# Optimization experiments

Measured on AMD Instinct MI355X. Metric: run time of the kernel, lower is better.

The kernel has to match this reference:

```python
import jax, jax.numpy as jnp
import numpy as np

EPS = 1e-5

# The 8 fixed sobel kernels from the original module. Summing convolutions with
# the same input equals one convolution with the summed kernel, so we embed the
# four 3x3 kernels (pad=1) into 5x5 (pad=2) and precombine everything into a
# single depthwise 5x5 kernel (exactly the math of detect_edge_1/2 summed).
_K3 = [
    [[2, 4, 2], [0, 0, 0], [-2, -4, -2]],
    [[4, 2, 0], [2, 0, -2], [0, -2, -4]],
    [[2, 0, -2], [4, 0, -4], [2, 0, -2]],
    [[0, -2, -4], [2, 0, -2], [4, 2, 0]],
]
_K5 = [
    [[0, 0, 0, 0, 0], [0, -2, -4, -2, 0], [-1, -4, 0, 4, 1], [0, 2, 4, 2, 0], [0, 0, 0, 0, 0]],
    [[0, 0, -1, 0, 0], [0, -2, -4, 2, 0], [0, -4, 0, 4, 0], [0, -2, 4, 2, 0], [0, 0, 1, 0, 0]],
    [[0, 0, 1, 0, 0], [0, -2, 4, 2, 0], [0, -4, 0, 4, 0], [0, -2, -4, 2, 0], [0, 0, -1, 0, 0]],
    [[0, 0, 0, 0, 0], [0, 2, 4, 2, 0], [-1, -4, 0, 4, 1], [0, -2, -4, -2, 0], [0, 0, 0, 0, 0]],
]

def _combined_sobel_kernel():
    k = np.zeros((5, 5), dtype=np.float32)
    for k3 in _K3:
        k[1:4, 1:4] += np.asarray(k3, dtype=np.float32)
    for k5 in _K5:
        k += np.asarray(k5, dtype=np.float32)
    return jnp.asarray(k)

SOBEL_K = _combined_sobel_kernel()  # [5,5]


def _conv2d(x, w, b, pad):
    # x: [N,C,H,W], w: [O,I,kh,kw]
    y = jax.lax.conv_general_dilated(
        x, w, window_strides=(1, 1), padding=[(pad, pad), (pad, pad)],
        dimension_numbers=('NCHW', 'OIHW', 'NCHW'))
    return y + b[None, :, None, None]


def _bn_relu(y, gamma, beta):
    # BatchNorm2d in training mode: per-channel batch stats over (N,H,W),
    # biased variance, eps=1e-5.
    m = jnp.mean(y, axis=(0, 2, 3), keepdims=True)
    v = jnp.mean(jnp.square(y - m), axis=(0, 2, 3), keepdims=True)
    yn = (y - m) * jax.lax.rsqrt(v + EPS)
    return jax.nn.relu(yn * gamma[None, :, None, None] + beta[None, :, None, None])


def _single_conv(x, w, b, gamma, beta, pad):
    return _bn_relu(_conv2d(x, w, b, pad), gamma, beta)


def _sobel(x):
    # Fused depthwise conv replacing the per-channel loops over 8 kernels.
    C = x.shape[1]
    w = jnp.broadcast_to(SOBEL_K[None, None], (C, 1, 5, 5))
    return jax.lax.conv_general_dilated(
        x, w, window_strides=(1, 1), padding=[(2, 2), (2, 2)],
        dimension_numbers=('NCHW', 'OIHW', 'NCHW'), feature_group_count=C)


def setup_inputs() -> dict:
    key = jax.random.key(0)
    ks = jax.random.split(key, 16)
    Cin, Cout = 64, 128
    Ch = Cout // 2
    B, H, W = 8, 160, 160
    s = 0.05
    d = {
        'input_f': jax.random.normal(ks[0], (B, Cin, H, W), jnp.float32),
        'w1': jax.random.normal(ks[1], (Cout, Cin, 1, 1), jnp.float32) * s,
        'b1': jnp.zeros((Cout,), jnp.float32),
        'g1': jnp.ones((Cout,), jnp.float32),
        'be1': jnp.zeros((Cout,), jnp.float32),
        'w2': jax.random.normal(ks[2], (Ch, Cout, 3, 3), jnp.float32) * s,
        'b2': jnp.zeros((Ch,), jnp.float32),
        'g2': jnp.ones((Ch,), jnp.float32),
        'be2': jnp.zeros((Ch,), jnp.float32),
        'w3': jax.random.normal(ks[3], (Ch, Ch, 3, 3), jnp.float32) * s,
        'b3': jnp.zeros((Ch,), jnp.float32),
        'g3': jnp.ones((Ch,), jnp.float32),
        'be3': jnp.zeros((Ch,), jnp.float32),
        'w4': jax.random.normal(ks[4], (Ch, Cin, 3, 3), jnp.float32) * s,
        'b4': jnp.zeros((Ch,), jnp.float32),
        'g4': jnp.ones((Ch,), jnp.float32),
        'be4': jnp.zeros((Ch,), jnp.float32),
    }
    return d


def reference(input_f, w1, b1, g1, be1, w2, b2, g2, be2, w3, b3, g3, be3, w4, b4, g4, be4):
    c1 = _single_conv(input_f, w1, b1, g1, be1, pad=0)   # [B,Cout,H,W]
    c2 = _single_conv(c1, w2, b2, g2, be2, pad=1)        # [B,Cout//2,H,W]
    edge = _sobel(c2)                                    # depthwise sobel sum
    c3 = _single_conv(edge, w3, b3, g3, be3, pad=1)
    skip = _single_conv(input_f, w4, b4, g4, be4, pad=1)
    return jnp.concatenate([skip, c3], axis=1)           # [B,Cout,H,W]
```

## Files before the change

kernel.cpp:

```cpp
#include <hip/hip_runtime.h>

typedef unsigned short u16;
typedef unsigned int u32;
typedef __attribute__((ext_vector_type(8))) short bf16x8;
typedef __attribute__((ext_vector_type(4))) float f32x4;

#define WD 160
#define HW 25600
#define NPIXF 204800.0f
#define BNEPS 1e-5f
#define SLOTB 6553600ll
#define BATB  13107200ll

__device__ __forceinline__ float bf2f(u16 u){ return __uint_as_float(((u32)u)<<16); }
__device__ __forceinline__ u16 f2bf(float f){ u32 x=__float_as_uint(f); return (u16)((x + 0x7FFFu + ((x>>16)&1u))>>16); }
__device__ __forceinline__ u32 pack2(float a,float b){ return (u32)f2bf(a) | ((u32)f2bf(b)<<16); }

__device__ __forceinline__ f32x4 MF(bf16x8 a, bf16x8 b, f32x4 c){
  return __builtin_amdgcn_mfma_f32_16x16x32_bf16(a, b, c, 0, 0, 0);
}
__device__ __forceinline__ void gload16(const void* g, void* l){
  __builtin_amdgcn_global_load_lds((const __attribute__((address_space(1))) void*)(g),
                                   (__attribute__((address_space(3))) void*)(l), 16, 0, 0);
}

__global__ __launch_bounds__(256) void k_prepw(
    const float* __restrict__ w1, const float* __restrict__ w2,
    const float* __restrict__ w3, const float* __restrict__ w4,
    u16* __restrict__ wp1, u16* __restrict__ wp2,
    u16* __restrict__ wp3, u16* __restrict__ wp4)
{
  int t = blockIdx.x*256 + threadIdx.x;
  if (t < 8192){
    int i = t&7, oc = (t>>3)&127, kc = (t>>10)&3, icb = t>>12;
    wp1[t] = f2bf(w1[oc*64 + icb*32 + kc*8 + i]);
  }
  int u = t - 8192;
  if (u >= 0 && u < 73728){
    int i = u&7, oc = (u>>3)&63, kc = (u>>9)&3, v = u>>11;
    int icb = (v*57)>>9; int tap = v - icb*9;
    wp2[u] = f2bf(w2[(oc*128 + icb*32 + kc*8 + i)*9 + tap]);
  }
  int u3 = t - (8192+73728);
  if (u3 >= 0 && u3 < 36864){
    int k = u3&31, oc = (u3>>5)&63, v = u3>>11;
    int icb = (v >= 9) ? 1 : 0; int tap = v - icb*9;
    wp3[u3] = f2bf(w3[(oc*64 + icb*32 + k)*9 + tap]);
    wp4[u3] = f2bf(w4[(oc*64 + icb*32 + k)*9 + tap]);
  }
}

__global__ __launch_bounds__(256,4) void k_conv1(
    const float* __restrict__ x, const u16* __restrict__ wp1,
    char* __restrict__ dout, float* __restrict__ stats, int nslot)
{
  __shared__ __align__(16) char Xs[16384];
  const int tid = threadIdx.x, lane = tid&63, w = tid>>6;
  const int l15 = lane&15, kc = lane>>4;
  int flat = blockIdx.x + 200*blockIdx.y;
  flat = (flat&7)*200 + (flat>>3);
  const int b = flat/200, bx = flat - b*200;
  const int px0 = bx*128;
  const float* xb = x + (size_t)b*64*HW;

#pragma unroll
  for (int q=0; q<4; ++q){
    int s = q*256 + tid;
    int px = s & 127, ck = (s>>7)&3, icb = s>>9;
    const float* pb = xb + (size_t)(icb*32 + ck*8)*HW + px0 + px;
    u32 w4[4];
#pragma unroll
    for (int j=0;j<4;++j)
      w4[j] = pack2(pb[(size_t)(2*j)*HW], pb[(size_t)(2*j+1)*HW]);
    *(uint4*)(Xs + icb*8192 + px*64 + ((ck ^ ((px>>1)&3))<<4))
        = make_uint4(w4[0],w4[1],w4[2],w4[3]);
  }
  __syncthreads();

  f32x4 acc[4][4];
  for (int t=0;t<4;++t) for (int o=0;o<4;++o) acc[t][o] = (f32x4){0.f,0.f,0.f,0.f};
  const int och = (w>>1)*64;
  int a1off[4];
  for (int t=0;t<4;++t){
    int px = (w&1)*64 + t*16 + l15;
    a1off[t] = px*64 + ((kc ^ ((px>>1)&3))<<4);
  }
#pragma unroll
  for (int icb=0; icb<2; ++icb){
    bf16x8 a[4], bw[4];
#pragma unroll
    for (int t=0;t<4;++t) a[t] = *(const bf16x8*)(Xs + icb*8192 + a1off[t]);
#pragma unroll
    for (int o=0;o<4;++o)
      bw[o] = *(const bf16x8*)(wp1 + ((size_t)(icb*4 + kc)*128 + och + o*16 + l15)*8);
#pragma unroll
    for (int t=0;t<4;++t)
#pragma unroll
      for (int o=0;o<4;++o)
        acc[t][o] = MF(a[t], bw[o], acc[t][o]);
  }

  u16* c1 = (u16*)(dout + (size_t)b*BATB);
  float sa[4]={0,0,0,0}, sq[4]={0,0,0,0};
  for (int t=0;t<4;++t){
    int pxb = px0 + (w&1)*64 + t*16 + kc*4;
    for (int o=0;o<4;++o){
      int oc = och + o*16 + l15;
#pragma unroll
      for (int r=0;r<4;++r){
        float v = acc[t][o][r];
        c1[(size_t)(pxb + r)*128 + oc] = f2bf(v);
        sa[o]+=v; sq[o]+=v*v;
      }
    }
  }
  const int slot = flat & (nslot-1);
  for (int o=0;o<4;++o){
    float s1_=sa[o], s2_=sq[o];
    s1_+=__shfl_xor(s1_,16); s2_+=__shfl_xor(s2_,16);
    s1_+=__shfl_xor(s1_,32); s2_+=__shfl_xor(s2_,32);
    if (lane < 16){
      float* p = stats + ((size_t)slot*128 + och + o*16 + l15)*4;
      atomicAdd(p, s1_); atomicAdd(p+1, s2_);
    }
  }
}

__global__ void k_fold23(const float* __restrict__ s2, const float* __restrict__ s3,
                         float* __restrict__ f23, int nslot){
  int t = threadIdx.x;
  const float* src = (t < 128) ? s2 : s3;
  int c = t & 127;
  float sm=0.f, sq=0.f;
  for (int s=0;s<nslot;++s){ const float* p = src + ((size_t)s*128 + c)*4; sm+=p[0]; sq+=p[1]; }
  f23[t*2] = sm; f23[t*2+1] = sq;
}

__global__ __launch_bounds__(256,4) void k_conv2(
    char* __restrict__ dout, const u16* __restrict__ wp2,
    const float* __restrict__ S0, const float* __restrict__ g1,
    const float* __restrict__ be1,
    float* __restrict__ statsO, int nslot)
{
  __shared__ __align__(16) char Xs[21760];
  __shared__ __align__(16) float scbi[128][2];
  const int tid = threadIdx.x, lane = tid&63, w = tid>>6;
  const int l15 = lane&15, kc = lane>>4;
  int flat = blockIdx.x + 5*(blockIdx.y + 20*blockIdx.z);
  flat = (flat&7)*100 + (flat>>3);
  const int b = flat/100; int r100 = flat - b*100;
  const int by = r100/5, bx = r100 - by*5;
  const int gx0 = bx*32, gy0 = by*8;
  const u16* c1raw = (const u16*)(dout + (size_t)b*BATB);
  u16* raw2 = (u16*)(dout + (size_t)b*BATB + SLOTB);

  if (tid < 128){
    float sm=0.f, sq=0.f;
    for (int s=0;s<nslot;++s){ const float* p = S0 + ((size_t)s*128 + tid)*4; sm+=p[0]; sq+=p[1]; }
    float m = sm/NPIXF;
    float v = sq/NPIXF - m*m;
    float sc = g1[tid]*rsqrtf(v + BNEPS);
    scbi[tid][0] = sc; scbi[tid][1] = be1[tid] - m*sc;
  }

  f32x4 acc[4][4];
  for (int t=0;t<4;++t) for (int o=0;o<4;++o) acc[t][o] = (f32x4){0.f,0.f,0.f,0.f};

  int xon[2][3];
  for (int h=0;h<2;++h) for (int dx=0;dx<3;++dx){
    int xi = l15 + h*16 + dx;
    xon[h][dx] = xi*64 + ((kc ^ ((xi>>1)&3))<<4);
  }

  __syncthreads();
  for (int icb=0; icb<4; ++icb){
    if (icb) __syncthreads();
    for (int s = tid; s < 1360; s += 256){
      int p = s>>2, sub = s&3;
      int yy = (int)(((u32)p*241u)>>13);
      int xi = p - yy*34;
      int gy = gy0 - 1 + yy, gx = gx0 - 1 + xi;
      int c = sub ^ ((xi>>1)&3);
      uint4 o4 = make_uint4(0,0,0,0);
      if ((unsigned)gy < 160u && (unsigned)gx < 160u){
        int cb = icb*32 + c*8;
        uint4 q = *(const uint4*)(c1raw + ((size_t)(gy*WD+gx)*128 + cb));
        u32 ww[4] = {q.x,q.y,q.z,q.w};
        u32 ro[4];
#pragma unroll
        for (int j=0;j<4;++j){
          float lo = bf2f((u16)(ww[j]&0xFFFFu)), hi = bf2f((u16)(ww[j]>>16));
          lo = fmaxf(0.f, lo*scbi[cb+2*j][0]   + scbi[cb+2*j][1]);
          hi = fmaxf(0.f, hi*scbi[cb+2*j+1][0] + scbi[cb+2*j+1][1]);
          ro[j] = pack2(lo, hi);
        }
        o4 = make_uint4(ro[0],ro[1],ro[2],ro[3]);
      }
      *(uint4*)(Xs + p*64 + sub*16) = o4;
    }
    __syncthreads();
#pragma unroll
    for (int tap=0; tap<9; ++tap){
      const int dy = tap/3, dx = tap - dy*3;
      bf16x8 a[4], bw[4];
#pragma unroll
      for (int o=0;o<4;++o)
        bw[o] = *(const bf16x8*)(wp2 + ((size_t)((icb*9 + tap)*4 + kc)*64 + o*16 + l15)*8);
#pragma unroll
      for (int t=0;t<4;++t)
        a[t] = *(const bf16x8*)(Xs + (2*w + (t>>1) + dy)*2176 + xon[t&1][dx]);
#pragma unroll
      for (int t=0;t<4;++t)
#pragma unroll
        for (int o=0;o<4;++o)
          acc[t][o] = MF(a[t], bw[o], acc[t][o]);
    }
  }

  float sa[4]={0,0,0,0}, sq[4]={0,0,0,0};
  for (int t=0;t<4;++t){
    int gy = gy0 + 2*w + (t>>1);
    int gxb = gx0 + (t&1)*16 + kc*4;
    for (int o=0;o<4;++o){
      int oc = o*16 + l15;
#pragma unroll
      for (int r=0;r<4;++r){
        float v = acc[t][o][r];
        raw2[(size_t)(gy*WD + gxb + r)*64 + oc] = f2bf(v);
        sa[o]+=v; sq[o]+=v*v;
      }
    }
  }
  int slot = flat & (nslot-1);
  for (int o=0;o<4;++o){
    float s1_=sa[o], s2_=sq[o];
    s1_+=__shfl_xor(s1_,16); s2_+=__shfl_xor(s2_,16);
    s1_+=__shfl_xor(s1_,32); s2_+=__shfl_xor(s2_,32);
    if (lane<16){
      float* p = statsO + ((size_t)slot*128 + o*16 + l15)*4;
      atomicAdd(p,s1_); atomicAdd(p+1,s2_);
    }
  }
}

__global__ __launch_bounds__(256) void k_sobel(
    char* __restrict__ dout, const float* __restrict__ S1,
    const float* __restrict__ g2, const float* __restrict__ be2,
    u16* __restrict__ edge_base, long ebstride, int nslot)
{
  __shared__ float ascS[8], abiS[8];
  int tid = threadIdx.x;
  int b = blockIdx.z, cb = blockIdx.y;
  if (tid < 64){
    int c = cb*8 + (tid&7);
    float sm=0.f, sq=0.f;
    for (int s = tid>>3; s < nslot; s += 8){
      const float* p = S1 + ((size_t)s*128 + c)*4;
      sm += p[0]; sq += p[1];
    }
    sm += __shfl_xor(sm, 8);  sq += __shfl_xor(sq, 8);
    sm += __shfl_xor(sm, 16); sq += __shfl_xor(sq, 16);
    sm += __shfl_xor(sm, 32); sq += __shfl_xor(sq, 32);
    if (tid < 8){
      float m = sm/NPIXF, v = sq/NPIXF - m*m;
      float sc = g2[c]*rsqrtf(v+BNEPS);
      ascS[tid] = sc; abiS[tid] = be2[c] - m*sc;
    }
  }
  __syncthreads();
  int px = blockIdx.x*256 + tid;
  int y = (int)(((u32)px*52429u)>>23);
  int x = px - y*WD;
  const u16* raw2 = (const u16*)(dout + (size_t)b*BATB + SLOTB);
  u16* edge = edge_base + (size_t)b*ebstride;
  float av[8] = {0,0,0,0,0,0,0,0};
  auto TAP = [&](int dy, int dx, float wt){
    int yy = y+dy, xx = x+dx;
    if ((unsigned)yy>=160u || (unsigned)xx>=160u) return;
    uint4 q = *(const uint4*)(raw2 + ((size_t)(yy*WD+xx)*64 + cb*8));
    u32 ww[4] = {q.x,q.y,q.z,q.w};
#pragma unroll
    for (int j=0;j<4;++j){
      float lo = bf2f((u16)(ww[j]&0xFFFFu)), hi = bf2f((u16)(ww[j]>>16));
      lo = fmaxf(0.f, lo*ascS[2*j]   + abiS[2*j]);
      hi = fmaxf(0.f, hi*ascS[2*j+1] + abiS[2*j+1]);
      av[2*j]   += wt*lo;
      av[2*j+1] += wt*hi;
    }
  };
  TAP(-1,-1,4.f); TAP(-1,0,4.f);
  TAP(0,-2,-2.f); TAP(0,-1,-8.f); TAP(0,1,8.f); TAP(0,2,2.f);
  TAP(1,0,-4.f);  TAP(1,1,-4.f);
  uint4 o;
  o.x = pack2(av[0],av[1]); o.y = pack2(av[2],av[3]);
  o.z = pack2(av[4],av[5]); o.w = pack2(av[6],av[7]);
  *(uint4*)(edge + ((size_t)px*64 + cb*8)) = o;
}

__global__ __launch_bounds__(256,2) void k_conv34(
    char* __restrict__ dout, const float* __restrict__ x,
    const u16* __restrict__ wp3, const u16* __restrict__ wp4,
    float* __restrict__ st3, float* __restrict__ st4,
    const u16* __restrict__ zeros, const u16* __restrict__ edge_base,
    long ebstride, int nslot, int mode)
{
  __shared__ __align__(16) char Xs[24576];
  const int tid = threadIdx.x, lane = tid&63, w = tid>>6;
  const int l15 = lane&15, kc = lane>>4;
  int b, job;
  if (mode == 2){ b = blockIdx.z>>1; job = blockIdx.z&1; }
  else          { b = blockIdx.z;    job = mode; }
  const int gx0 = blockIdx.x*32, gy0 = blockIdx.y*8;
  const u16* wp = job ? wp4 : wp3;
  float* statsO = job ? st4 : st3;
  float* out = job ? (float*)(dout + (size_t)b*BATB)
                   : (float*)(dout + (size_t)b*BATB + SLOTB);
  const float* xb = x + (size_t)b*64*HW;
  const u16* edge = edge_base + (size_t)b*ebstride;

  f32x4 acc[4][4];
  for (int m=0;m<4;++m) for (int t=0;t<4;++t) acc[m][t] = (f32x4){0.f,0.f,0.f,0.f};
  int xon[2][3];
  for (int h=0;h<2;++h) for (int dx=0;dx<3;++dx){
    int xi = l15 + h*16 + dx;
    xon[h][dx] = xi*64 + ((kc ^ ((xi>>1)&3))<<4);
  }

  for (int icb=0; icb<2; ++icb){
    if (icb) __syncthreads();
    if (job){
      for (int s = tid; s < 1600; s += 256){
        int s10 = (int)(((u32)s*6554u)>>16);
        int q = s - s10*10;
        int cp = (int)(((u32)s10*6554u)>>16);
        int yq = s10 - cp*10;
        int gy = gy0 - 1 + yq;
        int gxq = gx0 - 4 + q*4;
        float fa[4] = {0,0,0,0}, fb[4] = {0,0,0,0};
        if ((unsigned)gy < 160u){
          const float* pa = xb + (size_t)(icb*32 + cp*2)*HW + gy*WD + gxq;
          if (gxq >= 0 && gxq + 3 < 160){
            float4 va = *(const float4*)pa;
            float4 vb = *(const float4*)(pa + HW);
            fa[0]=va.x; fa[1]=va.y; fa[2]=va.z; fa[3]=va.w;
            fb[0]=vb.x; fb[1]=vb.y; fb[2]=vb.z; fb[3]=vb.w;
          } else {
#pragma unroll
            for (int e=0;e<4;++e){
              int gx = gxq + e;
              if ((unsigned)gx < 160u){ fa[e] = pa[e]; fb[e] = pa[e + HW]; }
            }
          }
        }
#pragma unroll
        for (int e=0;e<4;++e){
          int xi = gxq + e - (gx0 - 1);
          if ((unsigned)xi < 34u){
            int phys = (yq*34 + xi)*64 + (((cp>>2) ^ ((xi>>1)&3))<<4) + (cp&3)*4;
            *(u32*)(Xs + phys) = pack2(fa[e], fb[e]);
          }
        }
      }
    } else {
      for (int it=0; it<6; ++it){
        int s = it*256 + tid;
        int p = s>>2, sub = s&3;
        int yy = (int)(((u32)p*241u)>>13);
        int xi = p - yy*34;
        int gy = gy0-1+yy, gx = gx0-1+xi;
        int c = sub ^ ((xi>>1)&3);
        const u16* src = zeros + ((tid&63)<<3);
        if (p<340 && (unsigned)gy<160u && (unsigned)gx<160u)
          src = edge + ((size_t)(gy*WD+gx)*64 + icb*32 + c*8);
        gload16(src, Xs + (it*256 + (tid & ~63))*16);
      }
      asm volatile("s_waitcnt vmcnt(0)" ::: "memory");
    }
    __syncthreads();

#pragma unroll
    for (int tap=0; tap<9; ++tap){
      const int dy = tap/3, dx = tap - dy*3;
      bf16x8 a[4], bv[4];
#pragma unroll
      for (int m=0;m<4;++m)
        a[m] = *(const bf16x8*)(wp + ((size_t)((icb*9+tap)*64 + m*16 + l15)*32 + kc*8));
#pragma unroll
      for (int t=0;t<4;++t)
        bv[t] = *(const bf16x8*)(Xs + (2*w + (t>>1) + dy)*2176 + xon[t&1][dx]);
#pragma unroll
      for (int m=0;m<4;++m)
#pragma unroll
        for (int t=0;t<4;++t)
          acc[m][t] = MF(a[m], bv[t], acc[m][t]);
    }
  }

  float sa[4][4], sq[4][4];
  for (int m=0;m<4;++m) for (int r=0;r<4;++r){ sa[m][r]=0.f; sq[m][r]=0.f; }
  for (int m=0;m<4;++m){
    for (int t=0;t<4;++t){
      int gy = gy0 + 2*w + (t>>1);
      int gx = gx0 + (t&1)*16 + l15;
#pragma unroll
      for (int r=0;r<4;++r){
        float v = acc[m][t][r];
        out[(size_t)(m*16 + kc*4 + r)*HW + gy*WD + gx] = v;
        sa[m][r]+=v; sq[m][r]+=v*v;
      }
    }
  }
  int slot = (blockIdx.x + 5*(blockIdx.y + 20*blockIdx.z)) & (nslot-1);
  for (int m=0;m<4;++m)
    for (int r=0;r<4;++r){
      float s1_=sa[m][r], s2_=sq[m][r];
      s1_+=__shfl_xor(s1_,1); s2_+=__shfl_xor(s2_,1);
      s1_+=__shfl_xor(s1_,2); s2_+=__shfl_xor(s2_,2);
      s1_+=__shfl_xor(s1_,4); s2_+=__shfl_xor(s2_,4);
      s1_+=__shfl_xor(s1_,8); s2_+=__shfl_xor(s2_,8);
      if (l15==0){
        float* p = statsO + ((size_t)slot*128 + m*16 + kc*4 + r)*4;
        atomicAdd(p,s1_); atomicAdd(p+1,s2_);
      }
    }
}

__global__ __launch_bounds__(256) void k_bnrelu(
    float* __restrict__ io, const float* __restrict__ f23,
    const float* __restrict__ g3, const float* __restrict__ be3,
    const float* __restrict__ g4, const float* __restrict__ be4)
{
  size_t e = ((size_t)blockIdx.x*256 + threadIdx.x)*8;
  int cg = (int)((e/HW) & 127);
  float* p = io + (size_t)blockIdx.y*3276800 + e;
  float sm,sq,gg,bb;
  if (cg>=64){ int c=cg-64; sm=f23[c*2]; sq=f23[c*2+1]; gg=g3[c]; bb=be3[c]; }
  else       { sm=f23[(128+cg)*2]; sq=f23[(128+cg)*2+1]; gg=g4[cg]; bb=be4[cg]; }
  float m = sm/NPIXF;
  float v = sq/NPIXF - m*m;
  float sc = gg*rsqrtf(v + BNEPS);
  float bi = bb - m*sc;
  float4 a = *(float4*)p;
  float4 bq = *(float4*)(p+4);
  a.x=fmaxf(0.f,a.x*sc+bi); a.y=fmaxf(0.f,a.y*sc+bi);
  a.z=fmaxf(0.f,a.z*sc+bi); a.w=fmaxf(0.f,a.w*sc+bi);
  bq.x=fmaxf(0.f,bq.x*sc+bi); bq.y=fmaxf(0.f,bq.y*sc+bi);
  bq.z=fmaxf(0.f,bq.z*sc+bi); bq.w=fmaxf(0.f,bq.w*sc+bi);
  *(float4*)p = a;
  *(float4*)(p+4) = bq;
}

extern "C" void kernel_launch(void* const* d_in, const int* in_sizes, int n_in,
                              void* d_out, int out_size, void* d_ws, size_t ws_size,
                              hipStream_t stream)
{
  const float* x   = (const float*)d_in[0];
  const float* w1  = (const float*)d_in[1];
  const float* g1  = (const float*)d_in[3];
  const float* be1 = (const float*)d_in[4];
  const float* w2  = (const float*)d_in[5];
  const float* g2  = (const float*)d_in[7];
  const float* be2 = (const float*)d_in[8];
  const float* w3  = (const float*)d_in[9];
  const float* g3  = (const float*)d_in[11];
  const float* be3 = (const float*)d_in[12];
  const float* w4  = (const float*)d_in[13];
  const float* g4  = (const float*)d_in[15];
  const float* be4 = (const float*)d_in[16];
  (void)in_sizes; (void)n_in; (void)out_size;

  int nslot = 32;
  auto need = [&](int ns)->size_t{
    return (size_t)4*ns*128*4*4 + 4096 + (size_t)(8192+73728+36864+36864)*2 + 1024;
  };
  while (nslot > 1 && need(nslot) > ws_size) nslot >>= 1;
  if (need(nslot) > ws_size) return;

  char* ws = (char*)d_ws;
  float* S = (float*)ws;
  size_t stg = (size_t)nslot*128*4;
  float* S0=S, *S1=S+stg, *S2=S+2*stg, *S3=S+3*stg;
  float* F = S + 4*stg;
  u16* wp1 = (u16*)(F + 1024);
  u16* wp2 = wp1 + 8192;
  u16* wp3 = wp2 + 73728;
  u16* wp4 = wp3 + 36864;
  u16* zeros = wp4 + 36864;
  size_t base = need(nslot);
  bool bigWS = (ws_size >= base + 26214400ull);
  u16* edge_base; long ebstride;
  if (bigWS){ edge_base = (u16*)(ws + base); ebstride = 64L*HW; }
  else      { edge_base = (u16*)((char*)d_out + 3276800); ebstride = BATB/2; }

  hipMemsetAsync(S, 0, 4*stg*sizeof(float), stream);
  hipMemsetAsync(zeros, 0, 1024, stream);

  k_prepw<<<464, 256, 0, stream>>>(w1, w2, w3, w4, wp1, wp2, wp3, wp4);
  k_conv1<<<dim3(200,8), 256, 0, stream>>>(x, wp1, (char*)d_out, S0, nslot);
  k_conv2<<<dim3(5,20,8), 256, 0, stream>>>((char*)d_out, wp2, S0, g1, be1, S1, nslot);
  k_sobel<<<dim3(100,8,8), 256, 0, stream>>>((char*)d_out, S1, g2, be2,
                                             edge_base, ebstride, nslot);
  if (bigWS){
    k_conv34<<<dim3(5,20,16), 256, 0, stream>>>((char*)d_out, x, wp3, wp4, S2, S3,
                                                zeros, edge_base, ebstride, nslot, 2);
  } else {
    k_conv34<<<dim3(5,20,8), 256, 0, stream>>>((char*)d_out, x, wp3, wp4, S2, S3,
                                               zeros, edge_base, ebstride, nslot, 0);
    k_conv34<<<dim3(5,20,8), 256, 0, stream>>>((char*)d_out, x, wp3, wp4, S2, S3,
                                               zeros, edge_base, ebstride, nslot, 1);
  }
  k_fold23<<<1, 256, 0, stream>>>(S2, S3, F, nslot);
  k_bnrelu<<<dim3(1600,8), 256, 0, stream>>>((float*)d_out, F, g3, be3, g4, be4);
}
```

Measured before the change: 341.6 us.

## Fuse skip conv with sobel into one launch, run conv3 alone

Adds a combined kernel whose first 800 blocks compute the skip-branch 3x3 conv (conv4) from the fp32 input with MFMA and accumulate BN stats. The remaining blocks perform the sobel edge computation. Because neither job depends on the other, they run concurrently within a single grid, and the later conv34 launch then only handles conv3. This aims to fill the GPU better and hide the memory-bound sobel behind compute-bound conv work, at the cost of more code and a larger mixed-role grid. It applies only on the large-workspace path.

```diff
diff --git a/kernel.cpp b/kernel.cpp
--- a/kernel.cpp
+++ b/kernel.cpp
@@ -295,6 +295,166 @@
   o.x = pack2(av[0],av[1]); o.y = pack2(av[2],av[3]);
   o.z = pack2(av[4],av[5]); o.w = pack2(av[6],av[7]);
   *(uint4*)(edge + ((size_t)px*64 + cb*8)) = o;
+}
+
+__global__ __launch_bounds__(256,2) void k_skipsobel(
+    char* __restrict__ dout, const float* __restrict__ x,
+    const u16* __restrict__ wp4, float* __restrict__ st4,
+    const float* __restrict__ S1, const float* __restrict__ g2,
+    const float* __restrict__ be2,
+    u16* __restrict__ edge_base, long ebstride, int nslot)
+{
+  __shared__ __align__(16) char Xs[24576];
+  __shared__ float ascS[8], abiS[8];
+  const int tid = threadIdx.x;
+  const int bid = blockIdx.x;
+
+  if (bid < 800){
+    const int lane = tid&63, w = tid>>6, l15 = lane&15, kc = lane>>4;
+    const int b = bid/100; int r100 = bid - b*100;
+    const int by = r100/5, bx = r100 - by*5;
+    const int gx0 = bx*32, gy0 = by*8;
+    const float* xb = x + (size_t)b*64*HW;
+    float* out = (float*)(dout + (size_t)b*BATB);
+
+    f32x4 acc[4][4];
+    for (int m=0;m<4;++m) for (int t=0;t<4;++t) acc[m][t] = (f32x4){0.f,0.f,0.f,0.f};
+    int xon[2][3];
+    for (int h=0;h<2;++h) for (int dx=0;dx<3;++dx){
+      int xi = l15 + h*16 + dx;
+      xon[h][dx] = xi*64 + ((kc ^ ((xi>>1)&3))<<4);
+    }
+
+    for (int icb=0; icb<2; ++icb){
+      if (icb) __syncthreads();
+      for (int s = tid; s < 1600; s += 256){
+        int s10 = (int)(((u32)s*6554u)>>16);
+        int q = s - s10*10;
+        int cp = (int)(((u32)s10*6554u)>>16);
+        int yq = s10 - cp*10;
+        int gy = gy0 - 1 + yq;
+        int gxq = gx0 - 4 + q*4;
+        float fa[4] = {0,0,0,0}, fb[4] = {0,0,0,0};
+        if ((unsigned)gy < 160u){
+          const float* pa = xb + (size_t)(icb*32 + cp*2)*HW + gy*WD + gxq;
+          if (gxq >= 0 && gxq + 3 < 160){
+            float4 va = *(const float4*)pa;
+            float4 vb = *(const float4*)(pa + HW);
+            fa[0]=va.x; fa[1]=va.y; fa[2]=va.z; fa[3]=va.w;
+            fb[0]=vb.x; fb[1]=vb.y; fb[2]=vb.z; fb[3]=vb.w;
+          } else {
+#pragma unroll
+            for (int e=0;e<4;++e){
+              int gx = gxq + e;
+              if ((unsigned)gx < 160u){ fa[e] = pa[e]; fb[e] = pa[e + HW]; }
+            }
+          }
+        }
+#pragma unroll
+        for (int e=0;e<4;++e){
+          int xi = gxq + e - (gx0 - 1);
+          if ((unsigned)xi < 34u){
+            int phys = (yq*34 + xi)*64 + (((cp>>2) ^ ((xi>>1)&3))<<4) + (cp&3)*4;
+            *(u32*)(Xs + phys) = pack2(fa[e], fb[e]);
+          }
+        }
+      }
+      __syncthreads();
+
+#pragma unroll
+      for (int tap=0; tap<9; ++tap){
+        const int dy = tap/3, dx = tap - dy*3;
+        bf16x8 a[4], bv[4];
+#pragma unroll
+        for (int m=0;m<4;++m)
+          a[m] = *(const bf16x8*)(wp4 + ((size_t)((icb*9+tap)*64 + m*16 + l15)*32 + kc*8));
+#pragma unroll
+        for (int t=0;t<4;++t)
+          bv[t] = *(const bf16x8*)(Xs + (2*w + (t>>1) + dy)*2176 + xon[t&1][dx]);
+#pragma unroll
+        for (int m=0;m<4;++m)
+#pragma unroll
+          for (int t=0;t<4;++t)
+            acc[m][t] = MF(a[m], bv[t], acc[m][t]);
+      }
+    }
+
+    float sa[4][4], sq[4][4];
+    for (int m=0;m<4;++m) for (int r=0;r<4;++r){ sa[m][r]=0.f; sq[m][r]=0.f; }
+    for (int m=0;m<4;++m){
+      for (int t=0;t<4;++t){
+        int gy = gy0 + 2*w + (t>>1);
+        int gx = gx0 + (t&1)*16 + l15;
+#pragma unroll
+        for (int r=0;r<4;++r){
+          float v = acc[m][t][r];
+          out[(size_t)(m*16 + kc*4 + r)*HW + gy*WD + gx] = v;
+          sa[m][r]+=v; sq[m][r]+=v*v;
+        }
+      }
+    }
+    int slot = bid & (nslot-1);
+    for (int m=0;m<4;++m)
+      for (int r=0;r<4;++r){
+        float s1_=sa[m][r], s2_=sq[m][r];
+        s1_+=__shfl_xor(s1_,1); s2_+=__shfl_xor(s2_,1);
+        s1_+=__shfl_xor(s1_,2); s2_+=__shfl_xor(s2_,2);
+        s1_+=__shfl_xor(s1_,4); s2_+=__shfl_xor(s2_,4);
+        s1_+=__shfl_xor(s1_,8); s2_+=__shfl_xor(s2_,8);
+        if (l15==0){
+          float* p = st4 + ((size_t)slot*128 + m*16 + kc*4 + r)*4;
+          atomicAdd(p,s1_); atomicAdd(p+1,s2_);
+        }
+      }
+  } else {
+    int s2i = bid - 800;
+    int b = s2i/800; int r800 = s2i - b*800;
+    int cb = r800/100, bxx = r800 - cb*100;
+    if (tid < 64){
+      int c = cb*8 + (tid&7);
+      float sm=0.f, sq=0.f;
+      for (int s = tid>>3; s < nslot; s += 8){
+        const float* p = S1 + ((size_t)s*128 + c)*4;
+        sm += p[0]; sq += p[1];
+      }
+      sm += __shfl_xor(sm, 8);  sq += __shfl_xor(sq, 8);
+      sm += __shfl_xor(sm, 16); sq += __shfl_xor(sq, 16);
+      sm += __shfl_xor(sm, 32); sq += __shfl_xor(sq, 32);
+      if (tid < 8){
+        float m = sm/NPIXF, v = sq/NPIXF - m*m;
+        float sc = g2[c]*rsqrtf(v+BNEPS);
+        ascS[tid] = sc; abiS[tid] = be2[c] - m*sc;
+      }
+    }
+    __syncthreads();
+    int px = bxx*256 + tid;
+    int y = (int)(((u32)px*52429u)>>23);
+    int x2 = px - y*WD;
+    const u16* raw2 = (const u16*)(dout + (size_t)b*BATB + SLOTB);
+    u16* edge = edge_base + (size_t)b*ebstride;
+    float av[8] = {0,0,0,0,0,0,0,0};
+    auto TAP = [&](int dy, int dx, float wt){
+      int yy = y+dy, xx = x2+dx;
+      if ((unsigned)yy>=160u || (unsigned)xx>=160u) return;
+      uint4 q = *(const uint4*)(raw2 + ((size_t)(yy*WD+xx)*64 + cb*8));
+      u32 ww[4] = {q.x,q.y,q.z,q.w};
+#pragma unroll
+      for (int j=0;j<4;++j){
+        float lo = bf2f((u16)(ww[j]&0xFFFFu)), hi = bf2f((u16)(ww[j]>>16));
+        lo = fmaxf(0.f, lo*ascS[2*j]   + abiS[2*j]);
+        hi = fmaxf(0.f, hi*ascS[2*j+1] + abiS[2*j+1]);
+        av[2*j]   += wt*lo;
+        av[2*j+1] += wt*hi;
+      }
+    };
+    TAP(-1,-1,4.f); TAP(-1,0,4.f);
+    TAP(0,-2,-2.f); TAP(0,-1,-8.f); TAP(0,1,8.f); TAP(0,2,2.f);
+    TAP(1,0,-4.f);  TAP(1,1,-4.f);
+    uint4 o;
+    o.x = pack2(av[0],av[1]); o.y = pack2(av[2],av[3]);
+    o.z = pack2(av[4],av[5]); o.w = pack2(av[6],av[7]);
+    *(uint4*)(edge + ((size_t)px*64 + cb*8)) = o;
+  }
 }
 
 __global__ __launch_bounds__(256,2) void k_conv34(
@@ -498,12 +658,14 @@
   k_prepw<<<464, 256, 0, stream>>>(w1, w2, w3, w4, wp1, wp2, wp3, wp4);
   k_conv1<<<dim3(200,8), 256, 0, stream>>>(x, wp1, (char*)d_out, S0, nslot);
   k_conv2<<<dim3(5,20,8), 256, 0, stream>>>((char*)d_out, wp2, S0, g1, be1, S1, nslot);
-  k_sobel<<<dim3(100,8,8), 256, 0, stream>>>((char*)d_out, S1, g2, be2,
-                                             edge_base, ebstride, nslot);
   if (bigWS){
-    k_conv34<<<dim3(5,20,16), 256, 0, stream>>>((char*)d_out, x, wp3, wp4, S2, S3,
-                                                zeros, edge_base, ebstride, nslot, 2);
+    k_skipsobel<<<7200, 256, 0, stream>>>((char*)d_out, x, wp4, S3, S1, g2, be2,
+                                          edge_base, ebstride, nslot);
+    k_conv34<<<dim3(5,20,8), 256, 0, stream>>>((char*)d_out, x, wp3, wp4, S2, S3,
+                                               zeros, edge_base, ebstride, nslot, 0);
   } else {
+    k_sobel<<<dim3(100,8,8), 256, 0, stream>>>((char*)d_out, S1, g2, be2,
+                                               edge_base, ebstride, nslot);
     k_conv34<<<dim3(5,20,8), 256, 0, stream>>>((char*)d_out, x, wp3, wp4, S2, S3,
                                                zeros, edge_base, ebstride, nslot, 0);
     k_conv34<<<dim3(5,20,8), 256, 0, stream>>>((char*)d_out, x, wp3, wp4, S2, S3,
```

Result: slower. 355.6 us (+4.1%).

## Add row-based sobel kernel staging three input rows of all channels in LDS

Applied to the files above, without the earlier changes.

Adds a new sobel kernel where each block handles one output row across all 64 channels. It loads three padded input rows into 64KB of shared memory via global_load_lds, applies BN+ReLU on the fly, and writes channel-contiguous 16-byte outputs. This kernel is used when the large workspace path is available, replacing the per-channel-block sobel launch there. It uses a sparse 8-tap stencil, which assumes the combined kernel's nonzero taps, and the 64KB LDS footprint limits occupancy.

```diff
diff --git a/kernel.cpp b/kernel.cpp
--- a/kernel.cpp
+++ b/kernel.cpp
@@ -240,6 +240,72 @@
       float* p = statsO + ((size_t)slot*128 + o*16 + l15)*4;
       atomicAdd(p,s1_); atomicAdd(p+1,s2_);
     }
+  }
+}
+
+__global__ __launch_bounds__(256,2) void k_sobelrow(
+    char* __restrict__ dout, const float* __restrict__ S1,
+    const float* __restrict__ g2, const float* __restrict__ be2,
+    u16* __restrict__ edge_base, long ebstride,
+    const u16* __restrict__ zeros, int nslot)
+{
+  __shared__ __align__(16) char Xs[65536];
+  __shared__ float ascS[64], abiS[64];
+  const int tid = threadIdx.x;
+  const int y = blockIdx.x, b = blockIdx.y;
+
+  if (tid < 64){
+    float sm=0.f, sq=0.f;
+    for (int s=0;s<nslot;++s){ const float* p = S1 + ((size_t)s*128 + tid)*4; sm+=p[0]; sq+=p[1]; }
+    float m = sm/NPIXF, v = sq/NPIXF - m*m;
+    float sc = g2[tid]*rsqrtf(v + BNEPS);
+    ascS[tid] = sc; abiS[tid] = be2[tid] - m*sc;
+  }
+
+  const u16* raw2 = (const u16*)(dout + (size_t)b*BATB + SLOTB);
+#pragma unroll
+  for (int it=0; it<16; ++it){
+    int s = it*256 + tid;
+    int r = (s >= 2624) ? 2 : ((s >= 1312) ? 1 : 0);
+    int sl = s - r*1312;
+    int p = sl>>3, c8 = sl&7;
+    int yy = y - 1 + r, gx = p - 2;
+    const u16* src = zeros + ((tid&63)<<3);
+    if (s < 3936 && (unsigned)yy < 160u && (unsigned)gx < 160u)
+      src = raw2 + ((size_t)(yy*WD + gx)*64 + c8*8);
+    gload16(src, Xs + (it*256 + (tid & ~63))*16);
+  }
+  asm volatile("s_waitcnt vmcnt(0)" ::: "memory");
+  __syncthreads();
+
+  u16* edge = edge_base + (size_t)b*ebstride;
+#pragma unroll
+  for (int i=0; i<5; ++i){
+    int s = i*256 + tid;
+    int px = s>>3, c8 = s&7;
+    const int ch0 = c8*8;
+    float av[8] = {0,0,0,0,0,0,0,0};
+    auto TAP = [&](int dy, int dx, float wt){
+      int yy = y+dy, xx = px+dx;
+      if ((unsigned)yy>=160u || (unsigned)xx>=160u) return;
+      uint4 q = *(const uint4*)(Xs + (((1+dy)*1312 + (xx+2)*8 + c8)<<4));
+      u32 ww[4] = {q.x,q.y,q.z,q.w};
+#pragma unroll
+      for (int j=0;j<4;++j){
+        float lo = bf2f((u16)(ww[j]&0xFFFFu)), hi = bf2f((u16)(ww[j]>>16));
+        lo = fmaxf(0.f, lo*ascS[ch0+2*j]   + abiS[ch0+2*j]);
+        hi = fmaxf(0.f, hi*ascS[ch0+2*j+1] + abiS[ch0+2*j+1]);
+        av[2*j]   += wt*lo;
+        av[2*j+1] += wt*hi;
+      }
+    };
+    TAP(-1,-1,4.f); TAP(-1,0,4.f);
+    TAP(0,-2,-2.f); TAP(0,-1,-8.f); TAP(0,1,8.f); TAP(0,2,2.f);
+    TAP(1,0,-4.f);  TAP(1,1,-4.f);
+    uint4 o;
+    o.x = pack2(av[0],av[1]); o.y = pack2(av[2],av[3]);
+    o.z = pack2(av[4],av[5]); o.w = pack2(av[6],av[7]);
+    *(uint4*)(edge + ((size_t)(y*WD + px)*64 + c8*8)) = o;
   }
 }
 
@@ -498,12 +564,14 @@
   k_prepw<<<464, 256, 0, stream>>>(w1, w2, w3, w4, wp1, wp2, wp3, wp4);
   k_conv1<<<dim3(200,8), 256, 0, stream>>>(x, wp1, (char*)d_out, S0, nslot);
   k_conv2<<<dim3(5,20,8), 256, 0, stream>>>((char*)d_out, wp2, S0, g1, be1, S1, nslot);
-  k_sobel<<<dim3(100,8,8), 256, 0, stream>>>((char*)d_out, S1, g2, be2,
-                                             edge_base, ebstride, nslot);
   if (bigWS){
+    k_sobelrow<<<dim3(160,8), 256, 0, stream>>>((char*)d_out, S1, g2, be2,
+                                                edge_base, ebstride, zeros, nslot);
     k_conv34<<<dim3(5,20,16), 256, 0, stream>>>((char*)d_out, x, wp3, wp4, S2, S3,
                                                 zeros, edge_base, ebstride, nslot, 2);
   } else {
+    k_sobel<<<dim3(100,8,8), 256, 0, stream>>>((char*)d_out, S1, g2, be2,
+                                               edge_base, ebstride, nslot);
     k_conv34<<<dim3(5,20,8), 256, 0, stream>>>((char*)d_out, x, wp3, wp4, S2, S3,
                                                zeros, edge_base, ebstride, nslot, 0);
     k_conv34<<<dim3(5,20,8), 256, 0, stream>>>((char*)d_out, x, wp3, wp4, S2, S3,
```

Result: faster. 324.5 us (-5.0%).
